# Optimization experiments

Measured on AMD Instinct MI355X. Metric: run time of the kernel, lower is better.

The kernel has to match this reference:

```python
import jax, jax.numpy as jnp
from jax import lax
import numpy as np

NPOINT = 1024
NSAMPLE = 32
RADIUS = 0.1
BN_EPS = 1e-5


def setup_inputs() -> dict:
    key = jax.random.key(0)
    k1, k2, k3 = jax.random.split(key, 3)
    B, N, C = 8, 4096, 128
    C_in, C_out = C + 3, 256
    xyz = jax.random.uniform(k1, (B, N, 3), dtype=jnp.float32)
    features = jax.random.normal(k2, (B, N, C), dtype=jnp.float32)
    W = jax.random.normal(k3, (C_out, C_in), dtype=jnp.float32) * 0.05
    b = jnp.zeros((C_out,), jnp.float32)
    return {
        "xyz": xyz,
        "features": features,
        "W": W,
        "b": b,
        "bn_gamma": jnp.ones((C_in,), jnp.float32),
        "bn_beta": jnp.zeros((C_in,), jnp.float32),
        "bn_mean": jnp.zeros((C_in,), jnp.float32),
        "bn_var": jnp.ones((C_in,), jnp.float32),
    }


def furthest_point_sample(xyz, npoint):
    # xyz: (B, N, 3) -> idx (B, npoint) int32; matches CUDA kernel (starts at index 0)
    B, N, _ = xyz.shape

    def step(carry, _):
        mind, last = carry  # (B,N), (B,)
        p = jnp.take_along_axis(xyz, last[:, None, None], axis=1)  # (B,1,3)
        d = jnp.sum((xyz - p) ** 2, axis=-1)  # (B,N)
        mind = jnp.minimum(mind, d)
        nxt = jnp.argmax(mind, axis=-1).astype(jnp.int32)
        return (mind, nxt), nxt

    init = (jnp.full((B, N), 1e10, xyz.dtype), jnp.zeros((B,), jnp.int32))
    _, rest = lax.scan(step, init, None, length=npoint - 1)  # (npoint-1, B)
    idx = jnp.concatenate([jnp.zeros((1, B), jnp.int32), rest], axis=0)
    return idx.T  # (B, npoint)


def ball_query(xyz, new_xyz, radius, nsample):
    # first `nsample` points of xyz within radius of each new_xyz, padded with first hit
    B, N, _ = xyz.shape
    d2 = jnp.sum((new_xyz[:, :, None, :] - xyz[:, None, :, :]) ** 2, axis=-1)  # (B,S,N)
    valid = d2 < radius * radius
    score = jnp.where(valid, jnp.arange(N, dtype=jnp.int32), jnp.int32(N))  # (B,S,N)
    neg_vals, _ = lax.top_k(-score, nsample)  # smallest indices first
    idx = -neg_vals  # (B,S,K)
    first = idx[..., :1]  # centroid is always within radius of itself
    idx = jnp.where(idx >= N, first, idx)
    return idx


def reference(xyz, features, W, b, bn_gamma, bn_beta, bn_mean, bn_var):
    B = xyz.shape[0]
    fps_idx = furthest_point_sample(xyz, NPOINT)  # (B,S)
    new_xyz = jnp.take_along_axis(xyz, fps_idx[:, :, None], axis=1)  # (B,S,3)
    idx = ball_query(xyz, new_xyz, RADIUS, NSAMPLE)  # (B,S,K)
    bidx = jnp.arange(B)[:, None, None]
    g_xyz = xyz[bidx, idx] - new_xyz[:, :, None, :]  # (B,S,K,3) centered
    g_feat = features[bidx, idx]  # (B,S,K,C)
    x = jnp.concatenate([g_xyz, g_feat], axis=-1)  # (B,S,K,C+3) use_xyz=True
    # PointConv: BN (eval) -> ReLU -> 1x1 conv -> max over nsample
    x = (x - bn_mean) * (bn_gamma / jnp.sqrt(bn_var + BN_EPS)) + bn_beta
    x = jax.nn.relu(x)
    y = jnp.einsum('bskc,oc->bsko', x, W) + b  # (B,S,K,O)
    y = jnp.max(y, axis=2)  # (B,S,O)
    new_features = jnp.transpose(y, (0, 2, 1))  # (B,O,S) like torch layout
    return new_xyz, new_features
```

## Files before the change

### kernel.cpp

```cpp
#pragma clang fp contract(off)
#include <hip/hip_runtime.h>
#include <math.h>

#define N_PTS   4096
#define B_SZ    8
#define NPOINT  1024
#define NSAMPLE 32
#define C_FEAT  128
#define C_IN    131
#define C_OUT   256
#define R2      1e-2f

#define KT      5
#define NT      16
#define KPAD    168

typedef __attribute__((ext_vector_type(8))) short bf16x8;
typedef __attribute__((ext_vector_type(4))) float f32x4;
typedef __attribute__((ext_vector_type(2))) float v2f;

__device__ __forceinline__ unsigned short f2bf(float f) {
    unsigned u = __float_as_uint(f);
    return (unsigned short)((u + 0x7FFF + ((u >> 16) & 1)) >> 16);
}
__device__ __forceinline__ float bf2f(unsigned short h) {
    return __uint_as_float(((unsigned)h) << 16);
}

__device__ __forceinline__ v2f pk_add(v2f a, v2f b) {
    v2f d; asm("v_pk_add_f32 %0, %1, %2" : "=v"(d) : "v"(a), "v"(b)); return d;
}
__device__ __forceinline__ v2f pk_mul(v2f a, v2f b) {
    v2f d; asm("v_pk_mul_f32 %0, %1, %2" : "=v"(d) : "v"(a), "v"(b)); return d;
}

__global__ __launch_bounds__(64) void k_wtrans(const float* __restrict__ W,
                                               unsigned short* __restrict__ Wb_hi,
                                               unsigned short* __restrict__ Wb_lo) {
    const int blk  = blockIdx.x;
    const int kt   = blk / NT, nt = blk % NT;
    const int lane = threadIdx.x;
    const int o    = nt * 16 + (lane & 15);
    const int k0   = kt * 32 + (lane >> 4) * 8;
    const size_t base = ((size_t)blk * 64 + lane) * 8;
#pragma unroll
    for (int j = 0; j < 8; ++j) {
        int k = k0 + j;
        float v = 0.0f;
        if (k < C_IN) {
            int src = (k < C_FEAT) ? (k + 3) : (k - C_FEAT);
            v = W[o * C_IN + src];
        }
        unsigned short hh = f2bf(v);
        Wb_hi[base + j] = hh;
        Wb_lo[base + j] = f2bf(v - bf2f(hh));
    }
}

#define FPS_BLOCK 512
#define FPS_PPT   8

#define DPP_IMAX(x, ctrl, rmask)                                              \
    do {                                                                      \
        int _y = __builtin_amdgcn_update_dpp(x, x, ctrl, rmask, 0xf, false);  \
        x = (_y > x) ? _y : x;                                                \
    } while (0)

__global__ __launch_bounds__(FPS_BLOCK) void k_fps(const float* __restrict__ xyz,
                                                   float* __restrict__ new_xyz) {
    const int b    = blockIdx.x;
    const int t    = threadIdx.x;
    const int lane = t & 63;
    const int wid  = t >> 6;
    __shared__ float xl[N_PTS], yl[N_PTS], zl[N_PTS];
    __shared__ unsigned long long red[2][FPS_BLOCK / 64];

    const float* base = xyz + (size_t)b * N_PTS * 3;

    v2f nX[4], nY[4], nZ[4], M[4];

    const float4* b4 = (const float4*)(base + (size_t)t * (FPS_PPT * 3));
    float4 v[6];
#pragma unroll
    for (int i = 0; i < 6; ++i) v[i] = b4[i];
    const float* vf = (const float*)v;
#pragma unroll
    for (int p = 0; p < 4; ++p) {
        float x0 = vf[(2 * p) * 3 + 0], x1 = vf[(2 * p + 1) * 3 + 0];
        float y0 = vf[(2 * p) * 3 + 1], y1 = vf[(2 * p + 1) * 3 + 1];
        float z0 = vf[(2 * p) * 3 + 2], z1 = vf[(2 * p + 1) * 3 + 2];
        nX[p] = (v2f){-x0, -x1};
        nY[p] = (v2f){-y0, -y1};
        nZ[p] = (v2f){-z0, -z1};
        M[p]  = (v2f){1e10f, 1e10f};
        int gi = t * FPS_PPT + 2 * p;
        xl[gi] = x0; xl[gi + 1] = x1;
        yl[gi] = y0; yl[gi + 1] = y1;
        zl[gi] = z0; zl[gi + 1] = z1;
    }
    __syncthreads();

    float cx = xl[0], cy = yl[0], cz = zl[0];
    if (t == 0) {
        float* o = new_xyz + (size_t)b * NPOINT * 3;
        o[0] = cx; o[1] = cy; o[2] = cz;
    }

    for (int it = 1; it < NPOINT; ++it) {
        const v2f ccx = (v2f){cx, cx};
        const v2f ccy = (v2f){cy, cy};
        const v2f ccz = (v2f){cz, cz};
#pragma unroll
        for (int p = 0; p < 4; ++p) {
            v2f dx = pk_add(nX[p], ccx);
            v2f dy = pk_add(nY[p], ccy);
            v2f dz = pk_add(nZ[p], ccz);
            v2f xx = pk_mul(dx, dx);
            v2f yy = pk_mul(dy, dy);
            v2f zz = pk_mul(dz, dz);
            v2f d  = pk_add(pk_add(xx, yy), zz);
            M[p].x = fminf(M[p].x, d.x);
            M[p].y = fminf(M[p].y, d.y);
        }
        float a0 = fmaxf(M[0].x, M[0].y), a1 = fmaxf(M[1].x, M[1].y);
        float a2 = fmaxf(M[2].x, M[2].y), a3 = fmaxf(M[3].x, M[3].y);
        const float bestv = fmaxf(fmaxf(a0, a1), fmaxf(a2, a3));
        const int bb = __float_as_int(bestv);
        int r = bb;
        DPP_IMAX(r, 0x111, 0xf);
        DPP_IMAX(r, 0x112, 0xf);
        DPP_IMAX(r, 0x114, 0xf);
        DPP_IMAX(r, 0x118, 0xf);
        DPP_IMAX(r, 0x142, 0xa);
        DPP_IMAX(r, 0x143, 0xc);
        const int vmax = __builtin_amdgcn_readlane(r, 63);
        const unsigned long long em = __ballot(bb == vmax);
        const int l = __ffsll((unsigned long long)em) - 1;
        int selj = 0;
#pragma unroll
        for (int j = 7; j >= 0; --j) {
            int bits = __float_as_int((j & 1) ? M[j >> 1].y : M[j >> 1].x);
            selj = (bits == vmax) ? j : selj;
        }
        const int gidx = t * FPS_PPT + selj;
        const int widx = __builtin_amdgcn_readlane(gidx, l);
        if (lane == 0)
            red[it & 1][wid] = ((unsigned long long)(unsigned)vmax << 32)
                             | (unsigned)(N_PTS - 1 - widx);
        __syncthreads();
        const unsigned long long* rp = red[it & 1];
        unsigned long long k0 = rp[0], k1 = rp[1], k2 = rp[2], k3 = rp[3];
        unsigned long long k4 = rp[4], k5 = rp[5], k6 = rp[6], k7 = rp[7];
        unsigned long long b01 = k0 > k1 ? k0 : k1;
        unsigned long long b23 = k2 > k3 ? k2 : k3;
        unsigned long long b45 = k4 > k5 ? k4 : k5;
        unsigned long long b67 = k6 > k7 ? k6 : k7;
        unsigned long long b03 = b01 > b23 ? b01 : b23;
        unsigned long long b47 = b45 > b67 ? b45 : b67;
        unsigned long long best = b03 > b47 ? b03 : b47;
        const int idx = N_PTS - 1 - (int)(best & 0xFFFFull);
        cx = xl[idx]; cy = yl[idx]; cz = zl[idx];
        if (t == 0) {
            float* o = new_xyz + ((size_t)b * NPOINT + it) * 3;
            o[0] = cx; o[1] = cy; o[2] = cz;
        }
    }
}

__global__ __launch_bounds__(256) void k_ballquery(const float* __restrict__ xyz,
                                                   const float* __restrict__ new_xyz,
                                                   int* __restrict__ out_idx) {
    const int lane = threadIdx.x & 63;
    const int wid  = threadIdx.x >> 6;
    const int b    = blockIdx.y;
    const int s    = blockIdx.x * 4 + wid;

    const float* xb = xyz + (size_t)b * N_PTS * 3;
    const float* q  = new_xyz + ((size_t)b * NPOINT + s) * 3;
    float qx = q[0], qy = q[1], qz = q[2];
    int* ob = out_idx + ((size_t)b * NPOINT + s) * NSAMPLE;

    int total = 0, first = -1;
    const unsigned long long mlt = (1ull << lane) - 1ull;

    for (int ch = 0; ch < N_PTS / 64; ++ch) {
        int i = ch * 64 + lane;
        float x = xb[i * 3 + 0], y = xb[i * 3 + 1], z = xb[i * 3 + 2];
        float dx = qx - x, dy = qy - y, dz = qz - z;
        float d2 = ((dx * dx) + (dy * dy)) + (dz * dz);
        bool valid = d2 < R2;
        unsigned long long m = __ballot(valid);
        if (valid) {
            int pos = total + __popcll(m & mlt);
            if (pos < NSAMPLE) ob[pos] = i;
        }
        if (first < 0 && m != 0ull) first = ch * 64 + (__ffsll(m) - 1);
        total += __popcll(m);
        if (total >= NSAMPLE) break;
    }
    if (total < NSAMPLE) {
        if (lane >= total && lane < NSAMPLE) ob[lane] = first;
    }
}

__device__ __forceinline__ float bn_relu(float v, float mean, float scale, float beta) {
    float r = ((v - mean) * scale) + beta;
    return fmaxf(r, 0.0f);
}

__global__ __launch_bounds__(256) void k_group_gemm(
    const float* __restrict__ xyz, const float* __restrict__ feat,
    const float* __restrict__ new_xyz, const int* __restrict__ idx,
    const unsigned short* __restrict__ Wb_hi, const unsigned short* __restrict__ Wb_lo,
    const float* __restrict__ bias,
    const float* __restrict__ bn_g, const float* __restrict__ bn_b,
    const float* __restrict__ bn_m, const float* __restrict__ bn_v,
    float* __restrict__ out) {
    const int sx = blockIdx.x;
    const int s  = ((sx & 7) << 7) | (sx >> 3);
    const int b  = blockIdx.y;
    const int t  = threadIdx.x;
    const int lane = t & 63;
    const int w    = t >> 6;

    __shared__ unsigned short Xh[32][KPAD], Xl[32][KPAD];
    __shared__ float sc_l[C_IN], mn_l[C_IN], bt_l[C_IN];
    __shared__ int   idxs[NSAMPLE];
    __shared__ float nq[3];

    if (t < C_IN) {
        float g  = bn_g[t];
        float vv = bn_v[t] + 1e-5f;
        sc_l[t] = g / sqrtf(vv);
        mn_l[t] = bn_m[t];
        bt_l[t] = bn_b[t];
    }
    if (t < NSAMPLE) idxs[t] = idx[((size_t)b * NPOINT + s) * NSAMPLE + t];
    if (t < 3)       nq[t]   = new_xyz[((size_t)b * NPOINT + s) * 3 + t];
    __syncthreads();

    {
        const int ks = t & 31;
        const int qh = t >> 5;
        const float* frow = feat + ((size_t)b * N_PTS + idxs[ks]) * C_FEAT;
#pragma unroll
        for (int m = 0; m < 4; ++m) {
            int qq = m * 8 + qh;
            int c0 = qq * 4;
            float4 f = *(const float4*)&frow[c0];
            float v0 = bn_relu(f.x, mn_l[3 + c0 + 0], sc_l[3 + c0 + 0], bt_l[3 + c0 + 0]);
            float v1 = bn_relu(f.y, mn_l[3 + c0 + 1], sc_l[3 + c0 + 1], bt_l[3 + c0 + 1]);
            float v2 = bn_relu(f.z, mn_l[3 + c0 + 2], sc_l[3 + c0 + 2], bt_l[3 + c0 + 2]);
            float v3 = bn_relu(f.w, mn_l[3 + c0 + 3], sc_l[3 + c0 + 3], bt_l[3 + c0 + 3]);
            unsigned short h0 = f2bf(v0), h1 = f2bf(v1), h2 = f2bf(v2), h3 = f2bf(v3);
            uint2 hv, lv;
            hv.x = (unsigned)h0 | ((unsigned)h1 << 16);
            hv.y = (unsigned)h2 | ((unsigned)h3 << 16);
            lv.x = (unsigned)f2bf(v0 - bf2f(h0)) | ((unsigned)f2bf(v1 - bf2f(h1)) << 16);
            lv.y = (unsigned)f2bf(v2 - bf2f(h2)) | ((unsigned)f2bf(v3 - bf2f(h3)) << 16);
            *(uint2*)&Xh[ks][c0] = hv;
            *(uint2*)&Xl[ks][c0] = lv;
        }
    }
    if (t < 32) {
        const int row = t;
        const int id  = idxs[row];
        const float* p = xyz + ((size_t)b * N_PTS + id) * 3;
        uint4 z4 = {0u, 0u, 0u, 0u};
        uint4 hh = z4, ll = z4;
        unsigned short h[3];
#pragma unroll
        for (int d = 0; d < 3; ++d) {
            float g = p[d] - nq[d];
            float v = bn_relu(g, mn_l[d], sc_l[d], bt_l[d]);
            h[d] = f2bf(v);
            unsigned short lo = f2bf(v - bf2f(h[d]));
            if (d == 0) { hh.x |= h[d];                 ll.x |= lo; }
            if (d == 1) { hh.x |= (unsigned)h[d] << 16; ll.x |= (unsigned)lo << 16; }
            if (d == 2) { hh.y |= h[d];                 ll.y |= lo; }
        }
        *(uint4*)&Xh[row][128] = hh;  *(uint4*)&Xl[row][128] = ll;
        *(uint4*)&Xh[row][136] = z4;  *(uint4*)&Xl[row][136] = z4;
        *(uint4*)&Xh[row][144] = z4;  *(uint4*)&Xl[row][144] = z4;
        *(uint4*)&Xh[row][152] = z4;  *(uint4*)&Xl[row][152] = z4;
        *(uint4*)&Xh[row][160] = z4;  *(uint4*)&Xl[row][160] = z4;
    }
    __syncthreads();

    f32x4 zero = {0.f, 0.f, 0.f, 0.f};
    f32x4 acc[2][4];
#pragma unroll
    for (int m = 0; m < 2; ++m)
#pragma unroll
        for (int n = 0; n < 4; ++n) acc[m][n] = zero;

    const int r0 = lane & 15;
#pragma unroll
    for (int kt = 0; kt < KT; ++kt) {
        const int k0 = kt * 32 + (lane >> 4) * 8;
        bf16x8 a0h = *(const bf16x8*)&Xh[r0][k0];
        bf16x8 a1h = *(const bf16x8*)&Xh[16 + r0][k0];
        bf16x8 a0l = *(const bf16x8*)&Xl[r0][k0];
        bf16x8 a1l = *(const bf16x8*)&Xl[16 + r0][k0];
#pragma unroll
        for (int n = 0; n < 4; ++n) {
            const int nt = w * 4 + n;
            const size_t off = (((size_t)kt * NT + nt) * 64 + lane) * 8;
            bf16x8 bh = *(const bf16x8*)&Wb_hi[off];
            bf16x8 bl = *(const bf16x8*)&Wb_lo[off];
            acc[0][n] = __builtin_amdgcn_mfma_f32_16x16x32_bf16(a0h, bh, acc[0][n], 0, 0, 0);
            acc[1][n] = __builtin_amdgcn_mfma_f32_16x16x32_bf16(a1h, bh, acc[1][n], 0, 0, 0);
            acc[0][n] = __builtin_amdgcn_mfma_f32_16x16x32_bf16(a0l, bh, acc[0][n], 0, 0, 0);
            acc[1][n] = __builtin_amdgcn_mfma_f32_16x16x32_bf16(a1l, bh, acc[1][n], 0, 0, 0);
            acc[0][n] = __builtin_amdgcn_mfma_f32_16x16x32_bf16(a0h, bl, acc[0][n], 0, 0, 0);
            acc[1][n] = __builtin_amdgcn_mfma_f32_16x16x32_bf16(a1h, bl, acc[1][n], 0, 0, 0);
        }
    }

#pragma unroll
    for (int n = 0; n < 4; ++n) {
        float m0 = fmaxf(acc[0][n][0], acc[1][n][0]);
        float m1 = fmaxf(acc[0][n][1], acc[1][n][1]);
        float m2 = fmaxf(acc[0][n][2], acc[1][n][2]);
        float m3 = fmaxf(acc[0][n][3], acc[1][n][3]);
        float pm = fmaxf(fmaxf(m0, m1), fmaxf(m2, m3));
        pm = fmaxf(pm, __shfl_xor(pm, 16));
        pm = fmaxf(pm, __shfl_xor(pm, 32));
        if (lane < 16) {
            int o = (w * 4 + n) * 16 + lane;
            out[(size_t)b * C_OUT * NPOINT + (size_t)o * NPOINT + s] = pm + bias[o];
        }
    }
}

extern "C" void kernel_launch(void* const* d_in, const int* in_sizes, int n_in,
                              void* d_out, int out_size, void* d_ws, size_t ws_size,
                              hipStream_t stream) {
    const float* xyz  = (const float*)d_in[0];
    const float* feat = (const float*)d_in[1];
    const float* W    = (const float*)d_in[2];
    const float* bias = (const float*)d_in[3];
    const float* bn_g = (const float*)d_in[4];
    const float* bn_b = (const float*)d_in[5];
    const float* bn_m = (const float*)d_in[6];
    const float* bn_v = (const float*)d_in[7];

    float* new_xyz  = (float*)d_out;
    float* out_feat = (float*)d_out + (size_t)B_SZ * NPOINT * 3;

    int*            ws_idx = (int*)d_ws;
    unsigned short* Wb_hi  = (unsigned short*)((char*)d_ws + (size_t)B_SZ * NPOINT * NSAMPLE * sizeof(int));
    unsigned short* Wb_lo  = Wb_hi + (size_t)KT * NT * 64 * 8;

    hipLaunchKernelGGL(k_wtrans, dim3(KT * NT), dim3(64), 0, stream, W, Wb_hi, Wb_lo);
    hipLaunchKernelGGL(k_fps, dim3(B_SZ), dim3(FPS_BLOCK), 0, stream, xyz, new_xyz);
    hipLaunchKernelGGL(k_ballquery, dim3(NPOINT / 4, B_SZ), dim3(256), 0, stream,
                       xyz, new_xyz, ws_idx);
    hipLaunchKernelGGL(k_group_gemm, dim3(NPOINT, B_SZ), dim3(256), 0, stream,
                       xyz, feat, new_xyz, ws_idx, Wb_hi, Wb_lo, bias,
                       bn_g, bn_b, bn_m, bn_v, out_feat);
}
```

Baseline: 874.3 us.

## Halve FPS block size, fuse argmax index into DPP reduction, pack xyz in LDS

The furthest-point-sample kernel now runs 256 threads with 16 points each instead of 512 with 8, so the per-iteration cross-wave reduction spans 4 waves instead of 8. The wave-level reduction carries the argmax index alongside the value through the DPP steps, which removes the ballot/readlane/select search. Coordinates are stored as float4 in LDS so the centroid fetch is a single load. The trade-off is more registers per thread, a longer serial per-thread loop, and a doubled DPP shuffle count. Tie-breaking relies on the >= comparison in the DPP steps plus the low-index encoding in the block reduction.

```diff
diff --git a/kernel.cpp b/kernel.cpp
--- a/kernel.cpp
+++ b/kernel.cpp
@@ -57,13 +57,24 @@
     }
 }
 
-#define FPS_BLOCK 512
-#define FPS_PPT   8
-
-#define DPP_IMAX(x, ctrl, rmask)                                              \
-    do {                                                                      \
-        int _y = __builtin_amdgcn_update_dpp(x, x, ctrl, rmask, 0xf, false);  \
-        x = (_y > x) ? _y : x;                                                \
+#define FPS_BLOCK 256
+#define FPS_PPT   16
+#define FPS_NW    (FPS_BLOCK / 64)
+
+#define DPP_ARGMAX(vb, vi, ctrl, rmask)                                           \
+    do {                                                                          \
+        int _nb = __builtin_amdgcn_update_dpp(vb, vb, ctrl, rmask, 0xf, false);   \
+        int _ni = __builtin_amdgcn_update_dpp(vi, vi, ctrl, rmask, 0xf, false);   \
+        bool _g = (_nb >= vb);                                                    \
+        vb = _g ? _nb : vb;                                                       \
+        vi = _g ? _ni : vi;                                                       \
+    } while (0)
+
+#define CMB(ab, aj, bb_, bj_)                                                     \
+    do {                                                                          \
+        bool _g = ((bb_) > (ab));                                                 \
+        ab = _g ? (bb_) : (ab);                                                   \
+        aj = _g ? (bj_) : (aj);                                                   \
     } while (0)
 
 __global__ __launch_bounds__(FPS_BLOCK) void k_fps(const float* __restrict__ xyz,
@@ -72,20 +83,20 @@
     const int t    = threadIdx.x;
     const int lane = t & 63;
     const int wid  = t >> 6;
-    __shared__ float xl[N_PTS], yl[N_PTS], zl[N_PTS];
-    __shared__ unsigned long long red[2][FPS_BLOCK / 64];
+    __shared__ float4 xyzw[N_PTS];
+    __shared__ unsigned long long red[2][FPS_NW];
 
     const float* base = xyz + (size_t)b * N_PTS * 3;
 
-    v2f nX[4], nY[4], nZ[4], M[4];
+    v2f nX[8], nY[8], nZ[8], M[8];
 
     const float4* b4 = (const float4*)(base + (size_t)t * (FPS_PPT * 3));
-    float4 v[6];
-#pragma unroll
-    for (int i = 0; i < 6; ++i) v[i] = b4[i];
+    float4 v[12];
+#pragma unroll
+    for (int i = 0; i < 12; ++i) v[i] = b4[i];
     const float* vf = (const float*)v;
 #pragma unroll
-    for (int p = 0; p < 4; ++p) {
+    for (int p = 0; p < 8; ++p) {
         float x0 = vf[(2 * p) * 3 + 0], x1 = vf[(2 * p + 1) * 3 + 0];
         float y0 = vf[(2 * p) * 3 + 1], y1 = vf[(2 * p + 1) * 3 + 1];
         float z0 = vf[(2 * p) * 3 + 2], z1 = vf[(2 * p + 1) * 3 + 2];
@@ -94,13 +105,13 @@
         nZ[p] = (v2f){-z0, -z1};
         M[p]  = (v2f){1e10f, 1e10f};
         int gi = t * FPS_PPT + 2 * p;
-        xl[gi] = x0; xl[gi + 1] = x1;
-        yl[gi] = y0; yl[gi + 1] = y1;
-        zl[gi] = z0; zl[gi + 1] = z1;
+        xyzw[gi]     = (float4){x0, y0, z0, 0.0f};
+        xyzw[gi + 1] = (float4){x1, y1, z1, 0.0f};
     }
     __syncthreads();
 
-    float cx = xl[0], cy = yl[0], cz = zl[0];
+    float4 c4 = xyzw[0];
+    float cx = c4.x, cy = c4.y, cz = c4.z;
     if (t == 0) {
         float* o = new_xyz + (size_t)b * NPOINT * 3;
         o[0] = cx; o[1] = cy; o[2] = cz;
@@ -110,8 +121,9 @@
         const v2f ccx = (v2f){cx, cx};
         const v2f ccy = (v2f){cy, cy};
         const v2f ccz = (v2f){cz, cz};
-#pragma unroll
-        for (int p = 0; p < 4; ++p) {
+        int pb[8], pj[8];
+#pragma unroll
+        for (int p = 0; p < 8; ++p) {
             v2f dx = pk_add(nX[p], ccx);
             v2f dy = pk_add(nY[p], ccy);
             v2f dz = pk_add(nZ[p], ccz);
@@ -121,45 +133,39 @@
             v2f d  = pk_add(pk_add(xx, yy), zz);
             M[p].x = fminf(M[p].x, d.x);
             M[p].y = fminf(M[p].y, d.y);
-        }
-        float a0 = fmaxf(M[0].x, M[0].y), a1 = fmaxf(M[1].x, M[1].y);
-        float a2 = fmaxf(M[2].x, M[2].y), a3 = fmaxf(M[3].x, M[3].y);
-        const float bestv = fmaxf(fmaxf(a0, a1), fmaxf(a2, a3));
-        const int bb = __float_as_int(bestv);
-        int r = bb;
-        DPP_IMAX(r, 0x111, 0xf);
-        DPP_IMAX(r, 0x112, 0xf);
-        DPP_IMAX(r, 0x114, 0xf);
-        DPP_IMAX(r, 0x118, 0xf);
-        DPP_IMAX(r, 0x142, 0xa);
-        DPP_IMAX(r, 0x143, 0xc);
-        const int vmax = __builtin_amdgcn_readlane(r, 63);
-        const unsigned long long em = __ballot(bb == vmax);
-        const int l = __ffsll((unsigned long long)em) - 1;
-        int selj = 0;
-#pragma unroll
-        for (int j = 7; j >= 0; --j) {
-            int bits = __float_as_int((j & 1) ? M[j >> 1].y : M[j >> 1].x);
-            selj = (bits == vmax) ? j : selj;
-        }
-        const int gidx = t * FPS_PPT + selj;
-        const int widx = __builtin_amdgcn_readlane(gidx, l);
-        if (lane == 0)
-            red[it & 1][wid] = ((unsigned long long)(unsigned)vmax << 32)
-                             | (unsigned)(N_PTS - 1 - widx);
+            int bx = __float_as_int(M[p].x);
+            int by = __float_as_int(M[p].y);
+            bool g = by > bx;
+            pb[p] = g ? by : bx;
+            pj[p] = g ? (2 * p + 1) : (2 * p);
+        }
+        CMB(pb[0], pj[0], pb[1], pj[1]);
+        CMB(pb[2], pj[2], pb[3], pj[3]);
+        CMB(pb[4], pj[4], pb[5], pj[5]);
+        CMB(pb[6], pj[6], pb[7], pj[7]);
+        CMB(pb[0], pj[0], pb[2], pj[2]);
+        CMB(pb[4], pj[4], pb[6], pj[6]);
+        CMB(pb[0], pj[0], pb[4], pj[4]);
+        int vb = pb[0];
+        int vi = t * FPS_PPT + pj[0];
+        DPP_ARGMAX(vb, vi, 0x111, 0xf);
+        DPP_ARGMAX(vb, vi, 0x112, 0xf);
+        DPP_ARGMAX(vb, vi, 0x114, 0xf);
+        DPP_ARGMAX(vb, vi, 0x118, 0xf);
+        DPP_ARGMAX(vb, vi, 0x142, 0xa);
+        DPP_ARGMAX(vb, vi, 0x143, 0xc);
+        if (lane == 63)
+            red[it & 1][wid] = ((unsigned long long)(unsigned)vb << 32)
+                             | (unsigned)(N_PTS - 1 - vi);
         __syncthreads();
         const unsigned long long* rp = red[it & 1];
         unsigned long long k0 = rp[0], k1 = rp[1], k2 = rp[2], k3 = rp[3];
-        unsigned long long k4 = rp[4], k5 = rp[5], k6 = rp[6], k7 = rp[7];
         unsigned long long b01 = k0 > k1 ? k0 : k1;
         unsigned long long b23 = k2 > k3 ? k2 : k3;
-        unsigned long long b45 = k4 > k5 ? k4 : k5;
-        unsigned long long b67 = k6 > k7 ? k6 : k7;
-        unsigned long long b03 = b01 > b23 ? b01 : b23;
-        unsigned long long b47 = b45 > b67 ? b45 : b67;
-        unsigned long long best = b03 > b47 ? b03 : b47;
+        unsigned long long best = b01 > b23 ? b01 : b23;
         const int idx = N_PTS - 1 - (int)(best & 0xFFFFull);
-        cx = xl[idx]; cy = yl[idx]; cz = zl[idx];
+        float4 w4 = xyzw[idx];
+        cx = w4.x; cy = w4.y; cz = w4.z;
         if (t == 0) {
             float* o = new_xyz + ((size_t)b * NPOINT + it) * 3;
             o[0] = cx; o[1] = cy; o[2] = cz;
```

Result: faster. 807.0 us (-7.7%).
